# Kernel optimization log

Hardware: AMD Instinct MI355X
Metric: run time of the kernel (lower is better)

The kernel has to match this reference:

```python
import jax, jax.numpy as jnp
import numpy as np

HID = 1024; H = 16; D = 64; MB = 16; BASE_LR = 1.0; EPS = 1e-5
B, S = 4, 2048


def setup_inputs():
    key = jax.random.key(0)
    ks = jax.random.split(key, 8)
    w = lambda k, sh: jax.random.normal(k, sh, jnp.float32) * 0.02
    return {
        "x": jax.random.normal(ks[0], (B, S, HID), jnp.float32),
        "Wq": w(ks[1], (HID, HID)), "Wk": w(ks[2], (HID, HID)), "Wv": w(ks[3], (HID, HID)),
        "W_init": w(ks[4], (H, D, D)), "b_init": jnp.zeros((H, 1, D), jnp.float32),
        "ttt_w": jnp.ones((H, D), jnp.float32), "ttt_b": jnp.zeros((H, D), jnp.float32),
        "post_w": jnp.ones((HID,), jnp.float32), "post_b": jnp.zeros((HID,), jnp.float32),
        "lr_w": w(ks[5], (H, HID)), "lr_b": jnp.zeros((H,), jnp.float32),
        "token_idx_offset": jnp.zeros((MB,), jnp.float32),
        "Wg": w(ks[6], (HID, HID)), "Wo": w(ks[7], (HID, HID)),
    }


def _ln(z, g, b):
    # z: (B,H,M,D); g,b: (H,D), per-head LayerNorm over last dim
    mu = z.mean(-1, keepdims=True)
    var = ((z - mu) ** 2).mean(-1, keepdims=True)
    zn = (z - mu) * jax.lax.rsqrt(var + EPS)
    return zn * g[None, :, None, :] + b[None, :, None, :]


def _ln_vjp(x, go, g):
    # analytic LayerNorm VJP, vectorized over (B,H,M,D)
    mu = x.mean(-1, keepdims=True)
    var = ((x - mu) ** 2).mean(-1, keepdims=True)
    std = jnp.sqrt(var + EPS)
    xc = x - mu
    gxn = go * g[None, :, None, :]
    gvar = (gxn * xc).sum(-1, keepdims=True) * -0.5 * (var + EPS) ** (-1.5)
    gmu = (gxn * (-1.0 / std)).sum(-1, keepdims=True) + gvar * (-2.0 * xc).sum(-1, keepdims=True) / D
    return gxn / std + gvar * 2.0 * xc / D + gmu / D


def _forward(x, Wq, Wk, Wv, W_init, b_init, ttt_w, ttt_b, post_w, post_b, lr_w, lr_b, token_idx_offset, Wg, Wo):
    NMB = S // MB

    def heads(Wp):  # (B,S,HID) -> (NMB,B,H,MB,D)
        t = (x @ Wp.T).reshape(B, S, H, D).transpose(0, 2, 1, 3)
        return t.reshape(B, H, NMB, MB, D).transpose(2, 0, 1, 3, 4)

    Q, K, V = heads(Wq), heads(Wk), heads(Wv)

    # per-token, per-head learning rates
    lr_mult = jax.nn.sigmoid(jnp.einsum('bsd,hd->bhs', x, lr_w) + lr_b[None, :, None])
    lr_mult = lr_mult.reshape(B, H, NMB, MB, 1)
    token_idx = jnp.clip(1.0 / jnp.arange(1, MB + 1, dtype=jnp.float32) + token_idx_offset, 0.0)
    eta = BASE_LR * token_idx[None, None, None, :, None] * lr_mult / D
    eta = eta.transpose(2, 0, 1, 3, 4)  # (NMB,B,H,MB,1)

    tril1 = jnp.tril(jnp.ones((MB, MB), jnp.float32))

    def step(carry, xs):
        W, b = carry  # (H,D,D), (H,1,D)
        Qm, Km, Vm, em = xs  # (B,H,MB,D), em: (B,H,MB,1)
        Z = jnp.einsum('bhmd,hde->bhme', Km, W) + b[None]
        gZ = _ln_vjp(Z, _ln(Z, ttt_w, ttt_b) - (Vm - Km), ttt_w)
        Attn = jnp.tril(jnp.einsum('bhmd,bhnd->bhmn', Qm, Km))
        b_bar = b[None] - jnp.einsum('bhmn,bhnd->bhmd', em * tril1, gZ)
        Zb = jnp.einsum('bhmd,hde->bhme', Qm, W) - jnp.einsum('bhmn,bhnd->bhmd', em * Attn, gZ) + b_bar
        out = Qm + _ln(Zb, ttt_w, ttt_b)
        el = em[:, :, -1, :]  # (B,H,1)
        gl = gZ[:, :, -1, :]
        dW = jnp.einsum('bhd,bhe->hde', Km[:, :, -1, :], el * gl) / B
        db = jnp.mean(el * gl, axis=0)  # (H,D)
        return (W - dW, b - db[:, None, :]), out

    _, outs = jax.lax.scan(step, (W_init, b_init), (Q, K, V, eta))
    y = outs.transpose(1, 2, 0, 3, 4).reshape(B, H, S, D).transpose(0, 2, 1, 3).reshape(B, S, HID)
    mu = y.mean(-1, keepdims=True)
    var = ((y - mu) ** 2).mean(-1, keepdims=True)
    y = (y - mu) * jax.lax.rsqrt(var + EPS) * post_w + post_b
    gate = jax.nn.gelu(x @ Wg.T, approximate=False)
    return (gate * y) @ Wo.T


def reference(x, Wq, Wk, Wv, W_init, b_init, ttt_w, ttt_b, post_w, post_b, lr_w, lr_b, token_idx_offset, Wg, Wo):
    return _forward(x, Wq, Wk, Wv, W_init, b_init, ttt_w, ttt_b, post_w, post_b, lr_w, lr_b, token_idx_offset, Wg, Wo)
```

## Files before the change

### kernel.cpp

```cpp
#include <hip/hip_runtime.h>
#include <hip/hip_bf16.h>
#include <math.h>

typedef unsigned short u16;
typedef unsigned int u32;
typedef __attribute__((ext_vector_type(8))) short short8;
typedef __attribute__((ext_vector_type(4))) float f32x4;

#define MFMA16(a,b,c) __builtin_amdgcn_mfma_f32_16x16x32_bf16((a),(b),(c),0,0,0)

__device__ __forceinline__ u16 f2bf(float f) {
  u32 u = __float_as_uint(f);
  u32 r = (u + 0x7FFFu + ((u >> 16) & 1u)) >> 16;
  return (u16)r;
}
__device__ __forceinline__ float bf2f(u16 h) { return __uint_as_float(((u32)h) << 16); }
__device__ __forceinline__ void f2hl(float f, u16& h, u16& l) {
  h = f2bf(f);
  l = f2bf(f - bf2f(h));
}
__device__ __forceinline__ float wsum64(float v) {
#pragma unroll
  for (int off = 32; off > 0; off >>= 1) v += __shfl_xor(v, off, 64);
  return v;
}
__device__ __forceinline__ float wred64(float v) {
  v += __int_as_float(__builtin_amdgcn_update_dpp(0, __float_as_int(v), 0x111, 0xf, 0xf, true));
  v += __int_as_float(__builtin_amdgcn_update_dpp(0, __float_as_int(v), 0x112, 0xf, 0xf, true));
  v += __int_as_float(__builtin_amdgcn_update_dpp(0, __float_as_int(v), 0x114, 0xf, 0xf, true));
  v += __int_as_float(__builtin_amdgcn_update_dpp(0, __float_as_int(v), 0x118, 0xf, 0xf, true));
  v += __int_as_float(__builtin_amdgcn_update_dpp(0, __float_as_int(v), 0x142, 0xa, 0xf, true));
  v += __int_as_float(__builtin_amdgcn_update_dpp(0, __float_as_int(v), 0x143, 0xc, 0xf, true));
  return __int_as_float(__builtin_amdgcn_readlane(__float_as_int(v), 63));
}
__device__ __forceinline__ float rdlane(float v, int lane) {
  return __int_as_float(__builtin_amdgcn_readlane(__float_as_int(v), lane));
}
__device__ __forceinline__ short8 s8zero() {
  short8 v;
#pragma unroll
  for (int j = 0; j < 8; ++j) v[j] = 0;
  return v;
}

__global__ __launch_bounds__(256) void k_cast(
    const float* __restrict__ x, const float* __restrict__ Wq, const float* __restrict__ Wk,
    const float* __restrict__ Wv, const float* __restrict__ Wg, const float* __restrict__ lrw,
    const float* __restrict__ Wo, u16* __restrict__ xb, u16* __restrict__ Wcat, u16* __restrict__ Wob) {
  int c = blockIdx.x * 256 + threadIdx.x;
  float4 v = make_float4(0.f, 0.f, 0.f, 0.f);
  u16* dst;
  if (c < 2097152) {
    v = *(const float4*)(x + (size_t)c * 4);
    dst = xb + (size_t)c * 4;
  } else if (c < 2097152 + 1081344) {
    int c2 = c - 2097152;
    int base = c2 * 4;
    int nr = base >> 10, col = base & 1023;
    if (nr < 1024)      v = *(const float4*)(Wq  + (size_t)nr * 1024 + col);
    else if (nr < 2048) v = *(const float4*)(Wk  + (size_t)(nr - 1024) * 1024 + col);
    else if (nr < 3072) v = *(const float4*)(Wv  + (size_t)(nr - 2048) * 1024 + col);
    else if (nr < 4096) v = *(const float4*)(Wg  + (size_t)(nr - 3072) * 1024 + col);
    else if (nr < 4112) v = *(const float4*)(lrw + (size_t)(nr - 4096) * 1024 + col);
    dst = Wcat + (size_t)base;
  } else {
    int c2 = c - (2097152 + 1081344);
    v = *(const float4*)(Wo + (size_t)c2 * 4);
    dst = Wob + (size_t)c2 * 4;
  }
  ushort4 o;
  o.x = f2bf(v.x); o.y = f2bf(v.y); o.z = f2bf(v.z); o.w = f2bf(v.w);
  *(ushort4*)dst = o;
}

__device__ __forceinline__ void gemm_core(const u16* __restrict__ A, const u16* __restrict__ Bw,
                                          int bm, int bn, u16* sA, u16* sB, f32x4 acc[4][4]) {
  int tid = threadIdx.x;
  int lane = tid & 63, wid = tid >> 6;
  int fr = lane & 15, qd = lane >> 4;
  int wm = (wid & 1) * 64, wn = (wid >> 1) * 64;
#pragma unroll
  for (int i = 0; i < 4; ++i)
#pragma unroll
    for (int j = 0; j < 4; ++j) {
      f32x4 zz = {0.f, 0.f, 0.f, 0.f};
      acc[i][j] = zz;
    }
  for (int k0 = 0; k0 < 1024; k0 += 32) {
    __syncthreads();
#pragma unroll
    for (int cc = 0; cc < 2; ++cc) {
      int ch = tid + cc * 256;
      int row = ch >> 2, kp = (ch & 3) << 3;
      *(uint4*)(sA + row * 40 + kp) = *(const uint4*)(A + (size_t)(bm * 128 + row) * 1024 + k0 + kp);
      *(uint4*)(sB + row * 40 + kp) = *(const uint4*)(Bw + (size_t)(bn * 128 + row) * 1024 + k0 + kp);
    }
    __syncthreads();
    short8 af[4], bfr[4];
#pragma unroll
    for (int i = 0; i < 4; ++i) af[i] = *(const short8*)(sA + (wm + i * 16 + fr) * 40 + qd * 8);
#pragma unroll
    for (int j = 0; j < 4; ++j) bfr[j] = *(const short8*)(sB + (wn + j * 16 + fr) * 40 + qd * 8);
#pragma unroll
    for (int i = 0; i < 4; ++i)
#pragma unroll
      for (int j = 0; j < 4; ++j) acc[i][j] = MFMA16(af[i], bfr[j], acc[i][j]);
  }
}

__global__ __launch_bounds__(256) void k_gemm1(
    const u16* __restrict__ A, const u16* __restrict__ Bw,
    float* __restrict__ Qf, float* __restrict__ Kf, float* __restrict__ Vf,
    u16* __restrict__ gateb, float* __restrict__ eta,
    const float* __restrict__ lr_b, const float* __restrict__ tio) {
  __shared__ __align__(16) u16 sA[128 * 40];
  __shared__ __align__(16) u16 sB[128 * 40];
  int bm = blockIdx.x & 63, bn = blockIdx.x >> 6;
  f32x4 acc[4][4];
  gemm_core(A, Bw, bm, bn, sA, sB, acc);
  int tid = threadIdx.x, lane = tid & 63, wid = tid >> 6;
  int fr = lane & 15, qd = lane >> 4;
  int wm = (wid & 1) * 64, wn = (wid >> 1) * 64;
#pragma unroll
  for (int i = 0; i < 4; ++i) {
    int gr0 = bm * 128 + wm + i * 16 + qd * 4;
#pragma unroll
    for (int j = 0; j < 4; ++j) {
      int gc = bn * 128 + wn + j * 16 + fr;
      if (gc < 3072) {
        int p = gc >> 10, rem = gc & 1023, hd = rem >> 6, dd = rem & 63;
        float* dst = (p == 0) ? Qf : ((p == 1) ? Kf : Vf);
#pragma unroll
        for (int r = 0; r < 4; ++r) {
          int gr = gr0 + r;
          int b_ = gr >> 11, s = gr & 2047;
          dst[(((size_t)(b_ * 16 + hd)) * 2048 + s) * 64 + dd] = acc[i][j][r];
        }
      } else if (gc < 4096) {
        int j2 = gc - 3072;
#pragma unroll
        for (int r = 0; r < 4; ++r) {
          int gr = gr0 + r;
          float vv = acc[i][j][r];
          float gl = 0.5f * vv * (1.0f + erff(vv * 0.70710678118654752f));
          gateb[(size_t)gr * 1024 + j2] = f2bf(gl);
        }
      } else if (gc < 4112) {
        int hd = gc - 4096;
        float lb = lr_b[hd];
#pragma unroll
        for (int r = 0; r < 4; ++r) {
          int gr = gr0 + r;
          int b_ = gr >> 11, s = gr & 2047, m = s & 15;
          float lm = 1.0f / (1.0f + expf(-(acc[i][j][r] + lb)));
          float tok = fmaxf(1.0f / (float)(m + 1) + tio[m], 0.0f);
          eta[((size_t)(b_ * 16 + hd)) * 2048 + s] = tok * lm * 0.015625f;
        }
      }
    }
  }
}

__global__ __launch_bounds__(1024) void k_phaseA(
    const float* __restrict__ Kf, const float* __restrict__ Vf, const float* __restrict__ eta,
    const float* __restrict__ W_init, const float* __restrict__ b_init,
    const float* __restrict__ ttt_w, const float* __restrict__ ttt_b,
    float* __restrict__ Wseq, float* __restrict__ bseq) {
  __shared__ float pbuf[2][16][4][64];
  __shared__ float ush[2][4][64];
  int h = blockIdx.x;
  int tid = threadIdx.x, lane = tid & 63;
  int wu = __builtin_amdgcn_readfirstlane(tid >> 6);
  int wu4 = wu * 4;
  bool owner = (wu < 4);
  float Wreg[4];
#pragma unroll
  for (int i = 0; i < 4; ++i) Wreg[i] = W_init[(size_t)h * 4096 + (wu4 + i) * 64 + lane];
  float bcur = b_init[h * 64 + lane];
  float g = ttt_w[h * 64 + lane], tb = ttt_b[h * 64 + lane];
  const float* kb0 = Kf + (((size_t)(0 * 16 + h)) * 2048 + 15) * 64;
  const float* kb1 = Kf + (((size_t)(1 * 16 + h)) * 2048 + 15) * 64;
  const float* kb2 = Kf + (((size_t)(2 * 16 + h)) * 2048 + 15) * 64;
  const float* kb3 = Kf + (((size_t)(3 * 16 + h)) * 2048 + 15) * 64;
  const float* vbw = Vf + (((size_t)(wu * 16 + h)) * 2048 + 15) * 64;
  const float* erow = eta + ((size_t)(wu * 16 + h)) * 2048 + 15;

  float kc0 = kb0[lane], kc1 = kb1[lane], kc2 = kb2[lane], kc3 = kb3[lane];
  float kn0 = kb0[1024 + lane], kn1 = kb1[1024 + lane];
  float kn2 = kb2[1024 + lane], kn3 = kb3[1024 + lane];
  float vcur = 0.f, vnx = 0.f, ecur = 0.f, enx = 0.f;
  if (owner) {
    vcur = vbw[lane]; vnx = vbw[1024 + lane];
    ecur = erow[0]; enx = erow[16];
  }
  {
    float p0 = 0.f, p1 = 0.f, p2 = 0.f, p3 = 0.f;
#pragma unroll
    for (int i = 0; i < 4; ++i) {
      float wr = Wreg[i];
      p0 += rdlane(kc0, wu4 + i) * wr;
      p1 += rdlane(kc1, wu4 + i) * wr;
      p2 += rdlane(kc2, wu4 + i) * wr;
      p3 += rdlane(kc3, wu4 + i) * wr;
    }
    pbuf[0][wu][0][lane] = p0; pbuf[0][wu][1][lane] = p1;
    pbuf[0][wu][2][lane] = p2; pbuf[0][wu][3][lane] = p3;
  }
  __syncthreads();
  float zc = 0.f;
  if (owner) {
    float zs = 0.f;
#pragma unroll
    for (int w = 0; w < 16; ++w) zs += pbuf[0][w][wu][lane];
    zc = zs + bcur;
  }

  for (int n = 0; n < 128; ++n) {
    int bi = n & 1, pi = (n + 1) & 1;
    int nf = (n < 126) ? n + 2 : 127;
    size_t nfoff = (size_t)nf * 1024;
    float kf0 = kb0[nfoff + lane], kf1 = kb1[nfoff + lane];
    float kf2 = kb2[nfoff + lane], kf3 = kb3[nfoff + lane];
    float vfx = 0.f, efx = 0.f;
    if (owner) { vfx = vbw[nfoff + lane]; efx = erow[nf * 16]; }
    {
      float4 t4;
      t4.x = Wreg[0]; t4.y = Wreg[1]; t4.z = Wreg[2]; t4.w = Wreg[3];
      *(float4*)(Wseq + (((size_t)h * 128 + n) * 64 + lane) * 64 + wu4) = t4;
      if (wu == 0) bseq[((size_t)h * 128 + n) * 64 + lane] = bcur;
    }
    {
      float p0 = 0.f, p1 = 0.f, p2 = 0.f, p3 = 0.f;
#pragma unroll
      for (int i = 0; i < 4; ++i) {
        float wr = Wreg[i];
        p0 += rdlane(kn0, wu4 + i) * wr;
        p1 += rdlane(kn1, wu4 + i) * wr;
        p2 += rdlane(kn2, wu4 + i) * wr;
        p3 += rdlane(kn3, wu4 + i) * wr;
      }
      pbuf[pi][wu][0][lane] = p0; pbuf[pi][wu][1][lane] = p1;
      pbuf[pi][wu][2][lane] = p2; pbuf[pi][wu][3][lane] = p3;
    }
    float D0 = 0.f, D1 = 0.f, D2 = 0.f, D3 = 0.f;
    if (owner) {
      float kon = (wu == 0) ? kn0 : (wu == 1) ? kn1 : (wu == 2) ? kn2 : kn3;
      D0 = wred64(kon * kc0); D1 = wred64(kon * kc1);
      D2 = wred64(kon * kc2); D3 = wred64(kon * kc3);
      float kl = (wu == 0) ? kc0 : (wu == 1) ? kc1 : (wu == 2) ? kc2 : kc3;
      float s1 = wred64(zc), s2 = wred64(zc * zc);
      float mu = s1 * 0.015625f;
      float var = s2 * 0.015625f - mu * mu;
      float rstd = rsqrtf(var + 1e-5f);
      float xc = zc - mu;
      float ln = xc * rstd * g + tb;
      float go = ln - (vcur - kl);
      float gxn = go * g;
      float sa = wred64(gxn * xc), sb_ = wred64(gxn);
      float gvar = -0.5f * sa * rstd * rstd * rstd;
      float gmu = -sb_ * rstd;
      float gz = gxn * rstd + gvar * 2.0f * xc * 0.015625f + gmu * 0.015625f;
      ush[bi][wu][lane] = 0.25f * ecur * gz;
    }
    __syncthreads();
    float u0 = ush[bi][0][lane], u1 = ush[bi][1][lane];
    float u2 = ush[bi][2][lane], u3 = ush[bi][3][lane];
    if (owner) {
      float bnext = bcur - (u0 + u1 + u2 + u3);
      float zs = 0.f;
#pragma unroll
      for (int w = 0; w < 16; ++w) zs += pbuf[pi][w][wu][lane];
      zc = zs - (D0 * u0 + D1 * u1 + D2 * u2 + D3 * u3) + bnext;
      bcur = bnext;
    }
#pragma unroll
    for (int i = 0; i < 4; ++i) {
      float a = rdlane(kc0, wu4 + i) * u0 + rdlane(kc1, wu4 + i) * u1 +
                rdlane(kc2, wu4 + i) * u2 + rdlane(kc3, wu4 + i) * u3;
      Wreg[i] -= a;
    }
    kc0 = kn0; kc1 = kn1; kc2 = kn2; kc3 = kn3;
    kn0 = kf0; kn1 = kf1; kn2 = kf2; kn3 = kf3;
    vcur = vnx; vnx = vfx; ecur = enx; enx = efx;
  }
}

__global__ __launch_bounds__(256) void k_phaseB(
    const float* __restrict__ Qf, const float* __restrict__ Kf, const float* __restrict__ Vf,
    const float* __restrict__ eta, const float* __restrict__ Wseq, const float* __restrict__ bseq,
    const float* __restrict__ ttt_w, const float* __restrict__ ttt_b, float* __restrict__ yout) {
  __shared__ __align__(16) u16 WtH[64 * 72], WtL[64 * 72];
  __shared__ __align__(16) u16 gzH[4][64 * 24], gzL[4][64 * 24];
  __shared__ __align__(16) float At[4][16 * 20];
  __shared__ float bsh[64];
  int bx = blockIdx.x;
  int n = bx & 127, h = bx >> 7;
  int tid = threadIdx.x, lane = tid & 63, wv = tid >> 6;
  int fr = lane & 15, qd = lane >> 4;

  {
    int e = tid >> 2, d0 = (tid & 3) << 4;
    const float* src = Wseq + (((size_t)h * 128 + n) * 64 + e) * 64 + d0;
#pragma unroll
    for (int gsub = 0; gsub < 2; ++gsub) {
      u16 hb[8], lb_[8];
#pragma unroll
      for (int i = 0; i < 8; i += 4) {
        float4 v = *(const float4*)(src + gsub * 8 + i);
        f2hl(v.x, hb[i], lb_[i]);
        f2hl(v.y, hb[i + 1], lb_[i + 1]);
        f2hl(v.z, hb[i + 2], lb_[i + 2]);
        f2hl(v.w, hb[i + 3], lb_[i + 3]);
      }
      uint4 ph, pl;
      ph.x = hb[0] | ((u32)hb[1] << 16); ph.y = hb[2] | ((u32)hb[3] << 16);
      ph.z = hb[4] | ((u32)hb[5] << 16); ph.w = hb[6] | ((u32)hb[7] << 16);
      pl.x = lb_[0] | ((u32)lb_[1] << 16); pl.y = lb_[2] | ((u32)lb_[3] << 16);
      pl.z = lb_[4] | ((u32)lb_[5] << 16); pl.w = lb_[6] | ((u32)lb_[7] << 16);
      *(uint4*)(&WtH[e * 72 + d0 + gsub * 8]) = ph;
      *(uint4*)(&WtL[e * 72 + d0 + gsub * 8]) = pl;
    }
    if (tid < 64) bsh[tid] = bseq[((size_t)h * 128 + n) * 64 + tid];
  }
  __syncthreads();

  const size_t bh = (size_t)(wv * 16 + h);
  const float* Qp = Qf + (bh * 2048 + (size_t)n * 16) * 64;
  const float* Kp = Kf + (bh * 2048 + (size_t)n * 16) * 64;
  const float* Vp = Vf + (bh * 2048 + (size_t)n * 16) * 64;
  const float* ep = eta + bh * 2048 + n * 16;

  short8 qH[2], qL[2], kH[2], kL[2];
#pragma unroll
  for (int s = 0; s < 2; ++s) {
    const float* p1 = Qp + fr * 64 + s * 32 + qd * 8;
    const float* p2 = Kp + fr * 64 + s * 32 + qd * 8;
#pragma unroll
    for (int j = 0; j < 8; ++j) {
      u16 hb, lb_;
      f2hl(p1[j], hb, lb_); qH[s][j] = (short)hb; qL[s][j] = (short)lb_;
      f2hl(p2[j], hb, lb_); kH[s][j] = (short)hb; kL[s][j] = (short)lb_;
    }
  }

  f32x4 Zt[4];
#pragma unroll
  for (int t = 0; t < 4; ++t) {
    f32x4 a = {0.f, 0.f, 0.f, 0.f};
#pragma unroll
    for (int s = 0; s < 2; ++s) {
      short8 wH = *(const short8*)(&WtH[(t * 16 + fr) * 72 + s * 32 + qd * 8]);
      short8 wL = *(const short8*)(&WtL[(t * 16 + fr) * 72 + s * 32 + qd * 8]);
      a = MFMA16(kH[s], wH, a);
      a = MFMA16(kL[s], wH, a);
      a = MFMA16(kH[s], wL, a);
    }
    float bv = bsh[t * 16 + fr];
    a[0] += bv; a[1] += bv; a[2] += bv; a[3] += bv;
    Zt[t] = a;
  }
  f32x4 Atn = {0.f, 0.f, 0.f, 0.f};
#pragma unroll
  for (int s = 0; s < 2; ++s) {
    Atn = MFMA16(qH[s], kH[s], Atn);
    Atn = MFMA16(qL[s], kH[s], Atn);
    Atn = MFMA16(qH[s], kL[s], Atn);
  }

  float gw[4], gb[4];
#pragma unroll
  for (int t = 0; t < 4; ++t) {
    gw[t] = ttt_w[h * 64 + t * 16 + fr];
    gb[t] = ttt_b[h * 64 + t * 16 + fr];
  }
  float s1[4], s2[4];
#pragma unroll
  for (int r = 0; r < 4; ++r) {
    float a0 = Zt[0][r], a1 = Zt[1][r], a2 = Zt[2][r], a3 = Zt[3][r];
    s1[r] = a0 + a1 + a2 + a3;
    s2[r] = a0 * a0 + a1 * a1 + a2 * a2 + a3 * a3;
  }
#pragma unroll
  for (int off = 1; off <= 8; off <<= 1) {
#pragma unroll
    for (int r = 0; r < 4; ++r) {
      s1[r] += __shfl_xor(s1[r], off, 64);
      s2[r] += __shfl_xor(s2[r], off, 64);
    }
  }
  float mu[4], rstd[4];
#pragma unroll
  for (int r = 0; r < 4; ++r) {
    mu[r] = s1[r] * 0.015625f;
    float var = s2[r] * 0.015625f - mu[r] * mu[r];
    rstd[r] = rsqrtf(var + 1e-5f);
  }
  float xc[4][4], gxn[4][4];
  float s3[4] = {0, 0, 0, 0}, s4[4] = {0, 0, 0, 0}, s5[4] = {0, 0, 0, 0};
#pragma unroll
  for (int t = 0; t < 4; ++t) {
#pragma unroll
    for (int r = 0; r < 4; ++r) {
      float z = Zt[t][r];
      float x = z - mu[r];
      xc[t][r] = x;
      float ln = x * rstd[r] * gw[t] + gb[t];
      float vV = Vp[(qd * 4 + r) * 64 + t * 16 + fr];
      float vK = Kp[(qd * 4 + r) * 64 + t * 16 + fr];
      float go = ln - (vV - vK);
      float gx = go * gw[t];
      gxn[t][r] = gx;
      s3[r] += gx * x;
      s4[r] += gx;
      s5[r] += x;
    }
  }
#pragma unroll
  for (int off = 1; off <= 8; off <<= 1) {
#pragma unroll
    for (int r = 0; r < 4; ++r) {
      s3[r] += __shfl_xor(s3[r], off, 64);
      s4[r] += __shfl_xor(s4[r], off, 64);
      s5[r] += __shfl_xor(s5[r], off, 64);
    }
  }
  float gvar[4], gmu[4];
#pragma unroll
  for (int r = 0; r < 4; ++r) {
    float r3 = rstd[r] * rstd[r] * rstd[r];
    gvar[r] = -0.5f * s3[r] * r3;
    gmu[r] = -s4[r] * rstd[r] + gvar[r] * (-2.0f * s5[r]) * 0.015625f;
  }
#pragma unroll
  for (int t = 0; t < 4; ++t) {
    u16 hb[4], lb_[4];
#pragma unroll
    for (int r = 0; r < 4; ++r) {
      float gz = gxn[t][r] * rstd[r] + gvar[r] * 2.0f * xc[t][r] * 0.015625f + gmu[r] * 0.015625f;
      f2hl(gz, hb[r], lb_[r]);
    }
    uint2 ph, pl;
    ph.x = hb[0] | ((u32)hb[1] << 16); ph.y = hb[2] | ((u32)hb[3] << 16);
    pl.x = lb_[0] | ((u32)lb_[1] << 16); pl.y = lb_[2] | ((u32)lb_[3] << 16);
    *(uint2*)(&gzH[wv][(t * 16 + fr) * 24 + qd * 4]) = ph;
    *(uint2*)(&gzL[wv][(t * 16 + fr) * 24 + qd * 4]) = pl;
  }
  *(f32x4*)(&At[wv][fr * 20 + qd * 4]) = Atn;

  float em = ep[fr];
  short8 aH = s8zero(), aL = s8zero();
  if (qd < 2) {
#pragma unroll
    for (int j = 0; j < 8; ++j) {
      int nn = qd * 8 + j;
      float av = 0.0f;
      if (nn <= fr) av = em * (1.0f + At[wv][nn * 20 + fr]);
      u16 hb, lb_;
      f2hl(av, hb, lb_);
      aH[j] = (short)hb;
      aL[j] = (short)lb_;
    }
  }
  f32x4 Ob[4];
#pragma unroll
  for (int t = 0; t < 4; ++t) {
    f32x4 a = {0.f, 0.f, 0.f, 0.f};
#pragma unroll
    for (int s = 0; s < 2; ++s) {
      short8 wH = *(const short8*)(&WtH[(t * 16 + fr) * 72 + s * 32 + qd * 8]);
      short8 wL = *(const short8*)(&WtL[(t * 16 + fr) * 72 + s * 32 + qd * 8]);
      a = MFMA16(qH[s], wH, a);
      a = MFMA16(qL[s], wH, a);
      a = MFMA16(qH[s], wL, a);
    }
    short8 gH = s8zero(), gL = s8zero();
    if (qd < 2) {
      gH = *(const short8*)(&gzH[wv][(t * 16 + fr) * 24 + qd * 8]);
      gL = *(const short8*)(&gzL[wv][(t * 16 + fr) * 24 + qd * 8]);
    }
    f32x4 c = {0.f, 0.f, 0.f, 0.f};
    c = MFMA16(aH, gH, c);
    c = MFMA16(aL, gH, c);
    c = MFMA16(aH, gL, c);
    float bv = bsh[t * 16 + fr];
#pragma unroll
    for (int r = 0; r < 4; ++r) Ob[t][r] = a[r] - c[r] + bv;
  }
#pragma unroll
  for (int r = 0; r < 4; ++r) {
    float a0 = Ob[0][r], a1 = Ob[1][r], a2 = Ob[2][r], a3 = Ob[3][r];
    s1[r] = a0 + a1 + a2 + a3;
    s2[r] = a0 * a0 + a1 * a1 + a2 * a2 + a3 * a3;
  }
#pragma unroll
  for (int off = 1; off <= 8; off <<= 1) {
#pragma unroll
    for (int r = 0; r < 4; ++r) {
      s1[r] += __shfl_xor(s1[r], off, 64);
      s2[r] += __shfl_xor(s2[r], off, 64);
    }
  }
#pragma unroll
  for (int r = 0; r < 4; ++r) {
    mu[r] = s1[r] * 0.015625f;
    float var = s2[r] * 0.015625f - mu[r] * mu[r];
    rstd[r] = rsqrtf(var + 1e-5f);
  }
#pragma unroll
  for (int t = 0; t < 4; ++t) {
#pragma unroll
    for (int r = 0; r < 4; ++r) {
      float ln = (Ob[t][r] - mu[r]) * rstd[r] * gw[t] + gb[t];
      float qv = Qp[(qd * 4 + r) * 64 + t * 16 + fr];
      yout[((size_t)wv * 2048 + n * 16 + qd * 4 + r) * 1024 + h * 64 + t * 16 + fr] = qv + ln;
    }
  }
}

__global__ __launch_bounds__(256) void k_postln(
    const float* __restrict__ yf, const u16* __restrict__ gateb,
    const float* __restrict__ post_w, const float* __restrict__ post_b, u16* __restrict__ zb) {
  __shared__ float red[8];
  int row = blockIdx.x, tid = threadIdx.x;
  int lane = tid & 63, wid = tid >> 6;
  const float* yr = yf + (size_t)row * 1024;
  float4 v = *(const float4*)(yr + tid * 4);
  float s1 = v.x + v.y + v.z + v.w;
  float s2 = v.x * v.x + v.y * v.y + v.z * v.z + v.w * v.w;
  s1 = wsum64(s1);
  s2 = wsum64(s2);
  if (lane == 0) { red[wid] = s1; red[4 + wid] = s2; }
  __syncthreads();
  s1 = red[0] + red[1] + red[2] + red[3];
  s2 = red[4] + red[5] + red[6] + red[7];
  float mu = s1 * (1.0f / 1024.0f);
  float var = s2 * (1.0f / 1024.0f) - mu * mu;
  float rstd = rsqrtf(var + 1e-5f);
  float vals[4] = {v.x, v.y, v.z, v.w};
  u16 ov[4];
#pragma unroll
  for (int i = 0; i < 4; ++i) {
    int cc = tid * 4 + i;
    float yn = (vals[i] - mu) * rstd * post_w[cc] + post_b[cc];
    float gt = bf2f(gateb[(size_t)row * 1024 + cc]);
    ov[i] = f2bf(gt * yn);
  }
  ushort4 o;
  o.x = ov[0]; o.y = ov[1]; o.z = ov[2]; o.w = ov[3];
  *(ushort4*)(zb + (size_t)row * 1024 + tid * 4) = o;
}

__global__ __launch_bounds__(256) void k_gemm2(const u16* __restrict__ A, const u16* __restrict__ Bw,
                                               float* __restrict__ Out) {
  __shared__ __align__(16) u16 sA[128 * 40];
  __shared__ __align__(16) u16 sB[128 * 40];
  int bm = blockIdx.x & 63, bn = blockIdx.x >> 6;
  f32x4 acc[4][4];
  gemm_core(A, Bw, bm, bn, sA, sB, acc);
  int tid = threadIdx.x, lane = tid & 63, wid = tid >> 6;
  int fr = lane & 15, qd = lane >> 4;
  int wm = (wid & 1) * 64, wn = (wid >> 1) * 64;
#pragma unroll
  for (int i = 0; i < 4; ++i) {
    int gr0 = bm * 128 + wm + i * 16 + qd * 4;
#pragma unroll
    for (int j = 0; j < 4; ++j) {
      int gc = bn * 128 + wn + j * 16 + fr;
#pragma unroll
      for (int r = 0; r < 4; ++r) Out[(size_t)(gr0 + r) * 1024 + gc] = acc[i][j][r];
    }
  }
}

#define OFF_XB    ((size_t)0)
#define OFF_WCAT  ((size_t)16777216)
#define OFF_WOB   ((size_t)25427968)
#define OFF_Q     ((size_t)27525120)
#define OFF_K     ((size_t)61079552)
#define OFF_V     ((size_t)94633984)
#define OFF_GATE  ((size_t)128188416)
#define OFF_ETA   ((size_t)144965632)
#define OFF_WSEQ  ((size_t)145489920)
#define OFF_BSEQ  ((size_t)179044352)
#define OFF_Y     ((size_t)179568640)
#define OFF_ZB    ((size_t)213123072)

extern "C" void kernel_launch(void* const* d_in, const int* in_sizes, int n_in,
                              void* d_out, int out_size, void* d_ws, size_t ws_size,
                              hipStream_t stream) {
  const float* x    = (const float*)d_in[0];
  const float* Wq   = (const float*)d_in[1];
  const float* Wk   = (const float*)d_in[2];
  const float* Wv   = (const float*)d_in[3];
  const float* Wini = (const float*)d_in[4];
  const float* bini = (const float*)d_in[5];
  const float* ttw  = (const float*)d_in[6];
  const float* ttb  = (const float*)d_in[7];
  const float* pw   = (const float*)d_in[8];
  const float* pb   = (const float*)d_in[9];
  const float* lrw  = (const float*)d_in[10];
  const float* lrb  = (const float*)d_in[11];
  const float* tio  = (const float*)d_in[12];
  const float* Wg   = (const float*)d_in[13];
  const float* Wo   = (const float*)d_in[14];
  (void)in_sizes; (void)n_in; (void)out_size; (void)ws_size;
  float* out = (float*)d_out;
  char* ws = (char*)d_ws;
  u16* xb    = (u16*)(ws + OFF_XB);
  u16* Wcat  = (u16*)(ws + OFF_WCAT);
  u16* Wob   = (u16*)(ws + OFF_WOB);
  float* Qf  = (float*)(ws + OFF_Q);
  float* Kf  = (float*)(ws + OFF_K);
  float* Vf  = (float*)(ws + OFF_V);
  u16* gateb = (u16*)(ws + OFF_GATE);
  float* eta = (float*)(ws + OFF_ETA);
  float* Wsq = (float*)(ws + OFF_WSEQ);
  float* bsq = (float*)(ws + OFF_BSEQ);
  float* yf  = (float*)(ws + OFF_Y);
  u16* zbuf  = (u16*)(ws + OFF_ZB);

  hipLaunchKernelGGL(k_cast, dim3(13440), dim3(256), 0, stream, x, Wq, Wk, Wv, Wg, lrw, Wo, xb, Wcat, Wob);
  hipLaunchKernelGGL(k_gemm1, dim3(64 * 33), dim3(256), 0, stream, xb, Wcat, Qf, Kf, Vf, gateb, eta, lrb, tio);
  hipLaunchKernelGGL(k_phaseA, dim3(16), dim3(1024), 0, stream, Kf, Vf, eta, Wini, bini, ttw, ttb, Wsq, bsq);
  hipLaunchKernelGGL(k_phaseB, dim3(2048), dim3(256), 0, stream, Qf, Kf, Vf, eta, Wsq, bsq, ttw, ttb, yf);
  hipLaunchKernelGGL(k_postln, dim3(8192), dim3(256), 0, stream, yf, gateb, pw, pb, zbuf);
  hipLaunchKernelGGL(k_gemm2, dim3(64 * 8), dim3(256), 0, stream, zbuf, Wob, out);
}
```

Measured before the change: 494.8 us.

## Overlap sequential phase A with big projection GEMM via last-row precompute

A small pre-kernel computes only the last-token K, V and eta rows per mini-batch, which is all the sequential weight-update scan needs. The scan then runs in 16 blocks of a fused kernel whose other blocks run the full QKV/gate projection GEMM concurrently. The GEMM is retiled to 256x256 tiles with 1024-thread blocks. This hides the serial scan latency behind the GEMM, at the cost of recomputing the last-row projections and changing the GEMM's occupancy.

```diff
diff --git a/kernel.cpp b/kernel.cpp
--- a/kernel.cpp
+++ b/kernel.cpp
@@ -108,67 +108,90 @@
   }
 }
 
-__global__ __launch_bounds__(256) void k_gemm1(
-    const u16* __restrict__ A, const u16* __restrict__ Bw,
-    float* __restrict__ Qf, float* __restrict__ Kf, float* __restrict__ Vf,
-    u16* __restrict__ gateb, float* __restrict__ eta,
+__global__ __launch_bounds__(256) void k_lastrow(
+    const u16* __restrict__ xb, const u16* __restrict__ Wcat,
+    float* __restrict__ Klast, float* __restrict__ Vlast, float* __restrict__ etalast,
     const float* __restrict__ lr_b, const float* __restrict__ tio) {
   __shared__ __align__(16) u16 sA[128 * 40];
   __shared__ __align__(16) u16 sB[128 * 40];
-  int bm = blockIdx.x & 63, bn = blockIdx.x >> 6;
-  f32x4 acc[4][4];
-  gemm_core(A, Bw, bm, bn, sA, sB, acc);
+  int g = blockIdx.x;
+  int bm = g & 3, bn = g >> 2;
+  int bcol0 = (bn < 16) ? (1024 + bn * 128) : 4096;
   int tid = threadIdx.x, lane = tid & 63, wid = tid >> 6;
   int fr = lane & 15, qd = lane >> 4;
   int wm = (wid & 1) * 64, wn = (wid >> 1) * 64;
+  f32x4 acc[4][4];
+#pragma unroll
+  for (int i = 0; i < 4; ++i)
+#pragma unroll
+    for (int j = 0; j < 4; ++j) {
+      f32x4 zz = {0.f, 0.f, 0.f, 0.f};
+      acc[i][j] = zz;
+    }
+  for (int k0 = 0; k0 < 1024; k0 += 32) {
+    __syncthreads();
+#pragma unroll
+    for (int cc = 0; cc < 2; ++cc) {
+      int ch = tid + cc * 256;
+      int row = ch >> 2, kp = (ch & 3) << 3;
+      int r = bm * 128 + row;
+      int xrow = (r >> 7) * 2048 + (r & 127) * 16 + 15;
+      *(uint4*)(sA + row * 40 + kp) = *(const uint4*)(xb + (size_t)xrow * 1024 + k0 + kp);
+      *(uint4*)(sB + row * 40 + kp) = *(const uint4*)(Wcat + (size_t)(bcol0 + row) * 1024 + k0 + kp);
+    }
+    __syncthreads();
+    short8 af[4], bfr[4];
+#pragma unroll
+    for (int i = 0; i < 4; ++i) af[i] = *(const short8*)(sA + (wm + i * 16 + fr) * 40 + qd * 8);
+#pragma unroll
+    for (int j = 0; j < 4; ++j) bfr[j] = *(const short8*)(sB + (wn + j * 16 + fr) * 40 + qd * 8);
+#pragma unroll
+    for (int i = 0; i < 4; ++i)
+#pragma unroll
+      for (int j = 0; j < 4; ++j) acc[i][j] = MFMA16(af[i], bfr[j], acc[i][j]);
+  }
+  float tok15 = fmaxf(1.0f / 16.0f + tio[15], 0.0f);
 #pragma unroll
   for (int i = 0; i < 4; ++i) {
     int gr0 = bm * 128 + wm + i * 16 + qd * 4;
 #pragma unroll
     for (int j = 0; j < 4; ++j) {
-      int gc = bn * 128 + wn + j * 16 + fr;
-      if (gc < 3072) {
-        int p = gc >> 10, rem = gc & 1023, hd = rem >> 6, dd = rem & 63;
-        float* dst = (p == 0) ? Qf : ((p == 1) ? Kf : Vf);
+      if (bn < 16) {
+        int kv = bcol0 - 1024 + wn + j * 16 + fr;
+        int sel = kv >> 10, rem = kv & 1023, hd = rem >> 6, dd = rem & 63;
+        float* dst = sel ? Vlast : Klast;
 #pragma unroll
         for (int r = 0; r < 4; ++r) {
           int gr = gr0 + r;
-          int b_ = gr >> 11, s = gr & 2047;
-          dst[(((size_t)(b_ * 16 + hd)) * 2048 + s) * 64 + dd] = acc[i][j][r];
+          int b_ = gr >> 7, n = gr & 127;
+          dst[((size_t)(b_ * 16 + hd) * 128 + n) * 64 + dd] = acc[i][j][r];
         }
-      } else if (gc < 4096) {
-        int j2 = gc - 3072;
+      } else if (wn == 0 && j == 0) {
+        int hd = fr;
+        float lb = lr_b[hd];
 #pragma unroll
         for (int r = 0; r < 4; ++r) {
           int gr = gr0 + r;
-          float vv = acc[i][j][r];
-          float gl = 0.5f * vv * (1.0f + erff(vv * 0.70710678118654752f));
-          gateb[(size_t)gr * 1024 + j2] = f2bf(gl);
-        }
-      } else if (gc < 4112) {
-        int hd = gc - 4096;
-        float lb = lr_b[hd];
-#pragma unroll
-        for (int r = 0; r < 4; ++r) {
-          int gr = gr0 + r;
-          int b_ = gr >> 11, s = gr & 2047, m = s & 15;
+          int b_ = gr >> 7, n = gr & 127;
           float lm = 1.0f / (1.0f + expf(-(acc[i][j][r] + lb)));
-          float tok = fmaxf(1.0f / (float)(m + 1) + tio[m], 0.0f);
-          eta[((size_t)(b_ * 16 + hd)) * 2048 + s] = tok * lm * 0.015625f;
+          etalast[(size_t)(b_ * 16 + hd) * 128 + n] = tok15 * lm * 0.015625f;
         }
       }
     }
   }
 }
 
-__global__ __launch_bounds__(1024) void k_phaseA(
-    const float* __restrict__ Kf, const float* __restrict__ Vf, const float* __restrict__ eta,
+__device__ void phaseA_role(
+    char* smem, int h,
+    const float* __restrict__ Klast, const float* __restrict__ Vlast,
+    const float* __restrict__ etalast,
     const float* __restrict__ W_init, const float* __restrict__ b_init,
     const float* __restrict__ ttt_w, const float* __restrict__ ttt_b,
     float* __restrict__ Wseq, float* __restrict__ bseq) {
-  __shared__ float pbuf[2][16][4][64];
-  __shared__ float ush[2][4][64];
-  int h = blockIdx.x;
+  float* pb = (float*)smem;
+  float* us = (float*)(smem + 32768);
+#define PBUF(bf, w, b, l) pb[(((bf) * 16 + (w)) * 4 + (b)) * 64 + (l)]
+#define USH(bf, b, l) us[((bf) * 4 + (b)) * 64 + (l)]
   int tid = threadIdx.x, lane = tid & 63;
   int wu = __builtin_amdgcn_readfirstlane(tid >> 6);
   int wu4 = wu * 4;
@@ -178,20 +201,20 @@
   for (int i = 0; i < 4; ++i) Wreg[i] = W_init[(size_t)h * 4096 + (wu4 + i) * 64 + lane];
   float bcur = b_init[h * 64 + lane];
   float g = ttt_w[h * 64 + lane], tb = ttt_b[h * 64 + lane];
-  const float* kb0 = Kf + (((size_t)(0 * 16 + h)) * 2048 + 15) * 64;
-  const float* kb1 = Kf + (((size_t)(1 * 16 + h)) * 2048 + 15) * 64;
-  const float* kb2 = Kf + (((size_t)(2 * 16 + h)) * 2048 + 15) * 64;
-  const float* kb3 = Kf + (((size_t)(3 * 16 + h)) * 2048 + 15) * 64;
-  const float* vbw = Vf + (((size_t)(wu * 16 + h)) * 2048 + 15) * 64;
-  const float* erow = eta + ((size_t)(wu * 16 + h)) * 2048 + 15;
+  const float* kb0 = Klast + (size_t)(0 * 16 + h) * 128 * 64;
+  const float* kb1 = Klast + (size_t)(1 * 16 + h) * 128 * 64;
+  const float* kb2 = Klast + (size_t)(2 * 16 + h) * 128 * 64;
+  const float* kb3 = Klast + (size_t)(3 * 16 + h) * 128 * 64;
+  const float* vbw = Vlast + (size_t)(wu * 16 + h) * 128 * 64;
+  const float* erow = etalast + (size_t)(wu * 16 + h) * 128;
 
   float kc0 = kb0[lane], kc1 = kb1[lane], kc2 = kb2[lane], kc3 = kb3[lane];
-  float kn0 = kb0[1024 + lane], kn1 = kb1[1024 + lane];
-  float kn2 = kb2[1024 + lane], kn3 = kb3[1024 + lane];
+  float kn0 = kb0[64 + lane], kn1 = kb1[64 + lane];
+  float kn2 = kb2[64 + lane], kn3 = kb3[64 + lane];
   float vcur = 0.f, vnx = 0.f, ecur = 0.f, enx = 0.f;
   if (owner) {
-    vcur = vbw[lane]; vnx = vbw[1024 + lane];
-    ecur = erow[0]; enx = erow[16];
+    vcur = vbw[lane]; vnx = vbw[64 + lane];
+    ecur = erow[0]; enx = erow[1];
   }
   {
     float p0 = 0.f, p1 = 0.f, p2 = 0.f, p3 = 0.f;
@@ -203,26 +226,26 @@
       p2 += rdlane(kc2, wu4 + i) * wr;
       p3 += rdlane(kc3, wu4 + i) * wr;
     }
-    pbuf[0][wu][0][lane] = p0; pbuf[0][wu][1][lane] = p1;
-    pbuf[0][wu][2][lane] = p2; pbuf[0][wu][3][lane] = p3;
+    PBUF(0, wu, 0, lane) = p0; PBUF(0, wu, 1, lane) = p1;
+    PBUF(0, wu, 2, lane) = p2; PBUF(0, wu, 3, lane) = p3;
   }
   __syncthreads();
   float zc = 0.f;
   if (owner) {
     float zs = 0.f;
 #pragma unroll
-    for (int w = 0; w < 16; ++w) zs += pbuf[0][w][wu][lane];
+    for (int w = 0; w < 16; ++w) zs += PBUF(0, w, wu, lane);
     zc = zs + bcur;
   }
 
   for (int n = 0; n < 128; ++n) {
     int bi = n & 1, pi = (n + 1) & 1;
     int nf = (n < 126) ? n + 2 : 127;
-    size_t nfoff = (size_t)nf * 1024;
+    size_t nfoff = (size_t)nf * 64;
     float kf0 = kb0[nfoff + lane], kf1 = kb1[nfoff + lane];
     float kf2 = kb2[nfoff + lane], kf3 = kb3[nfoff + lane];
     float vfx = 0.f, efx = 0.f;
-    if (owner) { vfx = vbw[nfoff + lane]; efx = erow[nf * 16]; }
+    if (owner) { vfx = vbw[nfoff + lane]; efx = erow[nf]; }
     {
       float4 t4;
       t4.x = Wreg[0]; t4.y = Wreg[1]; t4.z = Wreg[2]; t4.w = Wreg[3];
@@ -239,8 +262,8 @@
         p2 += rdlane(kn2, wu4 + i) * wr;
         p3 += rdlane(kn3, wu4 + i) * wr;
       }
-      pbuf[pi][wu][0][lane] = p0; pbuf[pi][wu][1][lane] = p1;
-      pbuf[pi][wu][2][lane] = p2; pbuf[pi][wu][3][lane] = p3;
+      PBUF(pi, wu, 0, lane) = p0; PBUF(pi, wu, 1, lane) = p1;
+      PBUF(pi, wu, 2, lane) = p2; PBUF(pi, wu, 3, lane) = p3;
     }
     float D0 = 0.f, D1 = 0.f, D2 = 0.f, D3 = 0.f;
     if (owner) {
@@ -260,16 +283,16 @@
       float gvar = -0.5f * sa * rstd * rstd * rstd;
       float gmu = -sb_ * rstd;
       float gz = gxn * rstd + gvar * 2.0f * xc * 0.015625f + gmu * 0.015625f;
-      ush[bi][wu][lane] = 0.25f * ecur * gz;
+      USH(bi, wu, lane) = 0.25f * ecur * gz;
     }
     __syncthreads();
-    float u0 = ush[bi][0][lane], u1 = ush[bi][1][lane];
-    float u2 = ush[bi][2][lane], u3 = ush[bi][3][lane];
+    float u0 = USH(bi, 0, lane), u1 = USH(bi, 1, lane);
+    float u2 = USH(bi, 2, lane), u3 = USH(bi, 3, lane);
     if (owner) {
       float bnext = bcur - (u0 + u1 + u2 + u3);
       float zs = 0.f;
 #pragma unroll
-      for (int w = 0; w < 16; ++w) zs += pbuf[pi][w][wu][lane];
+      for (int w = 0; w < 16; ++w) zs += PBUF(pi, w, wu, lane);
       zc = zs - (D0 * u0 + D1 * u1 + D2 * u2 + D3 * u3) + bnext;
       bcur = bnext;
     }
@@ -282,6 +305,105 @@
     kc0 = kn0; kc1 = kn1; kc2 = kn2; kc3 = kn3;
     kn0 = kf0; kn1 = kf1; kn2 = kf2; kn3 = kf3;
     vcur = vnx; vnx = vfx; ecur = enx; enx = efx;
+  }
+#undef PBUF
+#undef USH
+}
+
+__device__ void gemm_role(
+    char* smem, int g,
+    const u16* __restrict__ A, const u16* __restrict__ Bw,
+    float* __restrict__ Qf, float* __restrict__ Kf, float* __restrict__ Vf,
+    u16* __restrict__ gateb, float* __restrict__ eta,
+    const float* __restrict__ lr_b, const float* __restrict__ tio) {
+  u16* sA = (u16*)smem;
+  u16* sB = (u16*)(smem + 20480);
+  int bm = g & 31, bn = g >> 5;
+  int tid = threadIdx.x, lane = tid & 63, wid = tid >> 6;
+  int fr = lane & 15, qd = lane >> 4;
+  int wm = (wid & 3) * 64, wn = (wid >> 2) * 64;
+  int srow = tid >> 2, kp = (tid & 3) << 3;
+  const u16* aSrc = A + (size_t)(bm * 256 + srow) * 1024 + kp;
+  const u16* bSrc = Bw + (size_t)(bn * 256 + srow) * 1024 + kp;
+  f32x4 acc[4][4];
+#pragma unroll
+  for (int i = 0; i < 4; ++i)
+#pragma unroll
+    for (int j = 0; j < 4; ++j) {
+      f32x4 zz = {0.f, 0.f, 0.f, 0.f};
+      acc[i][j] = zz;
+    }
+  for (int k0 = 0; k0 < 1024; k0 += 32) {
+    __syncthreads();
+    *(uint4*)(sA + srow * 40 + kp) = *(const uint4*)(aSrc + k0);
+    *(uint4*)(sB + srow * 40 + kp) = *(const uint4*)(bSrc + k0);
+    __syncthreads();
+    short8 af[4], bfr[4];
+#pragma unroll
+    for (int i = 0; i < 4; ++i) af[i] = *(const short8*)(sA + (wm + i * 16 + fr) * 40 + qd * 8);
+#pragma unroll
+    for (int j = 0; j < 4; ++j) bfr[j] = *(const short8*)(sB + (wn + j * 16 + fr) * 40 + qd * 8);
+#pragma unroll
+    for (int i = 0; i < 4; ++i)
+#pragma unroll
+      for (int j = 0; j < 4; ++j) acc[i][j] = MFMA16(af[i], bfr[j], acc[i][j]);
+  }
+#pragma unroll
+  for (int i = 0; i < 4; ++i) {
+    int gr0 = bm * 256 + wm + i * 16 + qd * 4;
+#pragma unroll
+    for (int j = 0; j < 4; ++j) {
+      int gc = bn * 256 + wn + j * 16 + fr;
+      if (gc < 3072) {
+        int p = gc >> 10, rem = gc & 1023, hd = rem >> 6, dd = rem & 63;
+        float* dst = (p == 0) ? Qf : ((p == 1) ? Kf : Vf);
+#pragma unroll
+        for (int r = 0; r < 4; ++r) {
+          int gr = gr0 + r;
+          int b_ = gr >> 11, s = gr & 2047;
+          dst[(((size_t)(b_ * 16 + hd)) * 2048 + s) * 64 + dd] = acc[i][j][r];
+        }
+      } else if (gc < 4096) {
+        int j2 = gc - 3072;
+#pragma unroll
+        for (int r = 0; r < 4; ++r) {
+          int gr = gr0 + r;
+          float vv = acc[i][j][r];
+          float gl = 0.5f * vv * (1.0f + erff(vv * 0.70710678118654752f));
+          gateb[(size_t)gr * 1024 + j2] = f2bf(gl);
+        }
+      } else if (gc < 4112) {
+        int hd = gc - 4096;
+        float lb = lr_b[hd];
+#pragma unroll
+        for (int r = 0; r < 4; ++r) {
+          int gr = gr0 + r;
+          int b_ = gr >> 11, s = gr & 2047, m = s & 15;
+          float lm = 1.0f / (1.0f + expf(-(acc[i][j][r] + lb)));
+          float tok = fmaxf(1.0f / (float)(m + 1) + tio[m], 0.0f);
+          eta[((size_t)(b_ * 16 + hd)) * 2048 + s] = tok * lm * 0.015625f;
+        }
+      }
+    }
+  }
+}
+
+__global__ __launch_bounds__(1024, 1) void k_fused(
+    const u16* __restrict__ xb, const u16* __restrict__ Wcat,
+    float* __restrict__ Qf, float* __restrict__ Kf, float* __restrict__ Vf,
+    u16* __restrict__ gateb, float* __restrict__ eta,
+    const float* __restrict__ lr_b, const float* __restrict__ tio,
+    const float* __restrict__ Klast, const float* __restrict__ Vlast,
+    const float* __restrict__ etalast,
+    const float* __restrict__ W_init, const float* __restrict__ b_init,
+    const float* __restrict__ ttt_w, const float* __restrict__ ttt_b,
+    float* __restrict__ Wseq, float* __restrict__ bseq) {
+  __shared__ __align__(16) char smem[40960];
+  if (blockIdx.x < 16) {
+    phaseA_role(smem, blockIdx.x, Klast, Vlast, etalast, W_init, b_init,
+                ttt_w, ttt_b, Wseq, bseq);
+  } else {
+    gemm_role(smem, blockIdx.x - 16, xb, Wcat, Qf, Kf, Vf, gateb, eta, lr_b, tio);
   }
 }
 
@@ -584,6 +706,9 @@
 #define OFF_BSEQ  ((size_t)179044352)
 #define OFF_Y     ((size_t)179568640)
 #define OFF_ZB    ((size_t)213123072)
+#define OFF_KL    OFF_ZB
+#define OFF_VL    (OFF_ZB + 2097152)
+#define OFF_EL    (OFF_ZB + 4194304)
 
 extern "C" void kernel_launch(void* const* d_in, const int* in_sizes, int n_in,
                               void* d_out, int out_size, void* d_ws, size_t ws_size,
@@ -618,10 +743,14 @@
   float* bsq = (float*)(ws + OFF_BSEQ);
   float* yf  = (float*)(ws + OFF_Y);
   u16* zbuf  = (u16*)(ws + OFF_ZB);
+  float* Klast   = (float*)(ws + OFF_KL);
+  float* Vlast   = (float*)(ws + OFF_VL);
+  float* etalast = (float*)(ws + OFF_EL);
 
   hipLaunchKernelGGL(k_cast, dim3(13440), dim3(256), 0, stream, x, Wq, Wk, Wv, Wg, lrw, Wo, xb, Wcat, Wob);
-  hipLaunchKernelGGL(k_gemm1, dim3(64 * 33), dim3(256), 0, stream, xb, Wcat, Qf, Kf, Vf, gateb, eta, lrb, tio);
-  hipLaunchKernelGGL(k_phaseA, dim3(16), dim3(1024), 0, stream, Kf, Vf, eta, Wini, bini, ttw, ttb, Wsq, bsq);
+  hipLaunchKernelGGL(k_lastrow, dim3(68), dim3(256), 0, stream, xb, Wcat, Klast, Vlast, etalast, lrb, tio);
+  hipLaunchKernelGGL(k_fused, dim3(560), dim3(1024), 0, stream, xb, Wcat, Qf, Kf, Vf, gateb, eta, lrb, tio,
+                     Klast, Vlast, etalast, Wini, bini, ttw, ttb, Wsq, bsq);
   hipLaunchKernelGGL(k_phaseB, dim3(2048), dim3(256), 0, stream, Qf, Kf, Vf, eta, Wsq, bsq, ttw, ttb, yf);
   hipLaunchKernelGGL(k_postln, dim3(8192), dim3(256), 0, stream, yf, gateb, pw, pb, zbuf);
   hipLaunchKernelGGL(k_gemm2, dim3(64 * 8), dim3(256), 0, stream, zbuf, Wob, out);
```

After: 397.7 us. 19.6% less time.
